# Kernel optimization log

Hardware: AMD Instinct MI355X
Metric: run time of the kernel (lower is better)

## Reference

```python
import jax, jax.numpy as jnp
import numpy as np

N_HEAD = 16
NEG_BIG = 1e10

def setup_inputs() -> dict:
    key = jax.random.key(0)
    k1, k2, k3 = jax.random.split(key, 3)
    B, S, D = 2, 2048, 1024
    x = jax.random.normal(k1, (B, S, D), dtype=jnp.float32)
    c_attn_w = jax.random.normal(k2, (D, 3 * D), dtype=jnp.float32) * 0.02
    c_attn_b = jnp.zeros((3 * D,), dtype=jnp.float32)
    c_proj_w = jax.random.normal(k3, (D, D), dtype=jnp.float32) * 0.02
    c_proj_b = jnp.zeros((D,), dtype=jnp.float32)
    return {"x": x, "c_attn_w": c_attn_w, "c_attn_b": c_attn_b,
            "c_proj_w": c_proj_w, "c_proj_b": c_proj_b}

def reference(x, c_attn_w, c_attn_b, c_proj_w, c_proj_b):
    B, S, D = x.shape
    H = N_HEAD
    hd = D // H
    # Conv1D c_attn: x @ W + b -> (B, S, 3D)
    qkv = x @ c_attn_w + c_attn_b
    q, k, v = jnp.split(qkv, 3, axis=-1)
    # split heads -> (B, H, S, hd)
    q = q.reshape(B, S, H, hd).transpose(0, 2, 1, 3)
    k = k.reshape(B, S, H, hd).transpose(0, 2, 1, 3)
    v = v.reshape(B, S, H, hd).transpose(0, 2, 1, 3)
    # QK^T with scale (scale=True)
    w = jnp.einsum('bhqd,bhkd->bhqk', q, k) / jnp.sqrt(jnp.float32(hd))
    # additive/multiplicative causal mask, exactly as source: w*b - 1e10*(1-b)
    b = jnp.tril(jnp.ones((S, S), dtype=w.dtype))
    w = w * b - NEG_BIG * (1.0 - b)
    w = jax.nn.softmax(w, axis=-1)
    a = jnp.einsum('bhqk,bhkd->bhqd', w, v)
    # merge heads -> (B, S, D)
    a = a.transpose(0, 2, 1, 3).reshape(B, S, D)
    # Conv1D c_proj
    a = a @ c_proj_w + c_proj_b
    # present = stack(key (as (B,H,S,hd)), value)
    present = jnp.stack((k, v))
    return (a, present)
```

## Files before the change

### kernel.cpp

```cpp
#include <hip/hip_runtime.h>
#include <hip/hip_bf16.h>
#include <string.h>

#define BB 2
#define SS 2048
#define DD 1024
#define NH 16
#define TT (BB * SS)
#define N3 (3 * DD)
#define A_SIZE (TT * DD)
#define PRESENT_HALF (BB * NH * SS * 64)
#define C2Q 0.18033688011112043f
#define NKT 32

typedef __attribute__((ext_vector_type(8))) short short8;
typedef __attribute__((ext_vector_type(4))) float floatx4;
typedef __attribute__((ext_vector_type(8))) unsigned short ushort8;

__device__ __forceinline__ unsigned short f2bf(float f) {
    union { float f; unsigned u; } v; v.f = f;
    unsigned r = v.u + 0x7fffu + ((v.u >> 16) & 1u);
    return (unsigned short)(r >> 16);
}
__device__ __forceinline__ unsigned pack2bf(float a, float b) {
    __hip_bfloat162 h = __float22bfloat162_rn(float2{a, b});
    unsigned u; memcpy(&u, &h, 4); return u;
}
__device__ __forceinline__ float bf2f(unsigned short u) {
    union { unsigned u; float f; } v; v.u = ((unsigned)u) << 16; return v.f;
}

__device__ __forceinline__ void async16(const unsigned short* g, unsigned short* lds) {
    __builtin_amdgcn_global_load_lds(
        (const __attribute__((address_space(1))) unsigned int*)g,
        (__attribute__((address_space(3))) unsigned int*)lds,
        16, 0, 0);
}

__global__ __launch_bounds__(256) void cast_x_kernel(const float* __restrict__ src,
                                                     unsigned short* __restrict__ dst) {
    int i = (blockIdx.x * 256 + threadIdx.x) * 8;
    float4 a = *(const float4*)(src + i);
    float4 b = *(const float4*)(src + i + 4);
    ushort8 o;
    o[0] = f2bf(a.x); o[1] = f2bf(a.y); o[2] = f2bf(a.z); o[3] = f2bf(a.w);
    o[4] = f2bf(b.x); o[5] = f2bf(b.y); o[6] = f2bf(b.z); o[7] = f2bf(b.w);
    *(ushort8*)(dst + i) = o;
}

__global__ __launch_bounds__(256) void transpose_cast_kernel(const float* __restrict__ src,
                                                             unsigned short* __restrict__ dst,
                                                             int R, int C) {
    __shared__ float tile[32][33];
    int c0 = blockIdx.x * 32, r0 = blockIdx.y * 32;
    int tx = threadIdx.x, ty = threadIdx.y;
    for (int i = ty; i < 32; i += 8)
        tile[i][tx] = src[(size_t)(r0 + i) * C + c0 + tx];
    __syncthreads();
    for (int i = ty; i < 32; i += 8)
        dst[(size_t)(c0 + i) * R + r0 + tx] = f2bf(tile[tx][i]);
}

__global__ __launch_bounds__(256)
void pv_kernel(const unsigned short* __restrict__ qkv,
               unsigned short* __restrict__ vT,
               float* __restrict__ out) {
    __shared__ unsigned short tile[64][72];
    const int bh = blockIdx.x, st = blockIdx.y;
    const int b = bh >> 4, h = bh & 15;
    const int tid = threadIdx.x;
    const int r = tid >> 2, c = (tid & 3) * 16;
    const size_t row = (size_t)(b * SS + st * 64 + r);

    const unsigned short* srcv = qkv + row * 3072 + 2048 + h * 64 + c;
    ushort8 v0 = *(const ushort8*)(srcv);
    ushort8 v1 = *(const ushort8*)(srcv + 8);
    *(ushort8*)(&tile[r][c])     = v0;
    *(ushort8*)(&tile[r][c + 8]) = v1;
    float* dv = out + A_SIZE + PRESENT_HALF + ((size_t)bh * SS + st * 64 + r) * 64 + c;
    float4 f;
    f = {bf2f(v0[0]), bf2f(v0[1]), bf2f(v0[2]), bf2f(v0[3])}; *(float4*)(dv)      = f;
    f = {bf2f(v0[4]), bf2f(v0[5]), bf2f(v0[6]), bf2f(v0[7])}; *(float4*)(dv + 4)  = f;
    f = {bf2f(v1[0]), bf2f(v1[1]), bf2f(v1[2]), bf2f(v1[3])}; *(float4*)(dv + 8)  = f;
    f = {bf2f(v1[4]), bf2f(v1[5]), bf2f(v1[6]), bf2f(v1[7])}; *(float4*)(dv + 12) = f;

    const unsigned short* srck = qkv + row * 3072 + 1024 + h * 64 + c;
    ushort8 k0 = *(const ushort8*)(srck);
    ushort8 k1 = *(const ushort8*)(srck + 8);
    float* dk = out + A_SIZE + ((size_t)bh * SS + st * 64 + r) * 64 + c;
    f = {bf2f(k0[0]), bf2f(k0[1]), bf2f(k0[2]), bf2f(k0[3])}; *(float4*)(dk)      = f;
    f = {bf2f(k0[4]), bf2f(k0[5]), bf2f(k0[6]), bf2f(k0[7])}; *(float4*)(dk + 4)  = f;
    f = {bf2f(k1[0]), bf2f(k1[1]), bf2f(k1[2]), bf2f(k1[3])}; *(float4*)(dk + 8)  = f;
    f = {bf2f(k1[4]), bf2f(k1[5]), bf2f(k1[6]), bf2f(k1[7])}; *(float4*)(dk + 12) = f;

    __syncthreads();
    const int d = tid >> 2, s0 = (tid & 3) * 16;
    unsigned short tmp[16];
    for (int e = 0; e < 16; ++e) tmp[e] = tile[s0 + e][d];
    unsigned short* dst = vT + ((size_t)bh * 64 + d) * SS + st * 64 + s0;
    *(int4*)(dst)     = *(const int4*)(tmp);
    *(int4*)(dst + 8) = *(const int4*)(tmp + 8);
}

__global__ __launch_bounds__(256, 3)
void gemm_kernel(const unsigned short* __restrict__ A,
                 const unsigned short* __restrict__ Bt,
                 const float* __restrict__ bias,
                 int mode,
                 unsigned short* __restrict__ out_bf,
                 float* __restrict__ out_f) {
    __shared__ unsigned short As3[3][8][512];
    __shared__ unsigned short Bs3[3][8][512];
    const int tid = threadIdx.x;
    const int wave = tid >> 6, lane = tid & 63;
    const int l15 = lane & 15, quad = lane >> 4;
    const int wm = wave >> 1, wn = wave & 1;
    const int t0 = blockIdx.y * 128;
    const int n0 = blockIdx.x * 128;

    floatx4 acc[4][4];
    #pragma unroll
    for (int i = 0; i < 4; ++i)
        #pragma unroll
        for (int j = 0; j < 4; ++j)
            #pragma unroll
            for (int e = 0; e < 4; ++e) acc[i][j][e] = 0.f;

    const unsigned short* gA = A  + (size_t)(t0 + wave * 32 + l15) * 1024 + quad * 8;
    const unsigned short* gB = Bt + (size_t)(n0 + wave * 32 + l15) * 1024 + quad * 8;

    #define STAGE(buf_, koff_) {                                        \
        async16(gA + (koff_),             &As3[buf_][wave * 2][0]);     \
        async16(gA + (koff_) + 16 * 1024, &As3[buf_][wave * 2 + 1][0]); \
        async16(gB + (koff_),             &Bs3[buf_][wave * 2][0]);     \
        async16(gB + (koff_) + 16 * 1024, &Bs3[buf_][wave * 2 + 1][0]); }

    STAGE(0, 0);
    STAGE(1, 32);
    asm volatile("s_waitcnt vmcnt(4)" ::: "memory");
    __builtin_amdgcn_s_barrier();
    asm volatile("" ::: "memory");

    int cur = 0, nx2 = 2;
    for (int t = 0; t < NKT; ++t) {
        if (t < NKT - 2) STAGE(nx2, (t + 2) * 32);

        const unsigned short* aB = &As3[cur][wm * 4][0] + lane * 8;
        const unsigned short* bB = &Bs3[cur][wn * 4][0] + lane * 8;
        short8 af[4], bfr[4];
        #pragma unroll
        for (int mt = 0; mt < 4; ++mt) af[mt]  = *(const short8*)(aB + mt * 512);
        #pragma unroll
        for (int nt = 0; nt < 4; ++nt) bfr[nt] = *(const short8*)(bB + nt * 512);

        __builtin_amdgcn_s_setprio(1);
        #pragma unroll
        for (int mt = 0; mt < 4; ++mt)
            #pragma unroll
            for (int nt = 0; nt < 4; ++nt)
                acc[mt][nt] = __builtin_amdgcn_mfma_f32_16x16x32_bf16(bfr[nt], af[mt], acc[mt][nt], 0, 0, 0);
        __builtin_amdgcn_s_setprio(0);

        asm volatile("s_waitcnt lgkmcnt(0)" ::: "memory");
        if (t < NKT - 2) { asm volatile("s_waitcnt vmcnt(4)" ::: "memory"); }
        else             { asm volatile("s_waitcnt vmcnt(0)" ::: "memory"); }
        asm volatile("" ::: "memory");
        __builtin_amdgcn_s_barrier();
        asm volatile("" ::: "memory");

        cur = (cur == 2) ? 0 : cur + 1;
        nx2 = (nx2 == 2) ? 0 : nx2 + 1;
    }
    #undef STAGE

    const float qs = (mode == 0 && n0 < 1024) ? C2Q : 1.0f;
    #pragma unroll
    for (int mt = 0; mt < 4; ++mt) {
        const int t = t0 + wm * 64 + mt * 16 + l15;
        if (mode == 0) {
            unsigned short* po = out_bf + (size_t)t * 3072 + n0 + wn * 64;
            #pragma unroll
            for (int nt = 0; nt < 4; ++nt) {
                float4 b4 = *(const float4*)(bias + n0 + wn * 64 + nt * 16 + quad * 4);
                float v0 = (acc[mt][nt][0] + b4.x) * qs;
                float v1 = (acc[mt][nt][1] + b4.y) * qs;
                float v2 = (acc[mt][nt][2] + b4.z) * qs;
                float v3 = (acc[mt][nt][3] + b4.w) * qs;
                uint2 w = {pack2bf(v0, v1), pack2bf(v2, v3)};
                *(uint2*)(po + nt * 16 + quad * 4) = w;
            }
        } else {
            float* po = out_f + (size_t)t * 1024 + n0 + wn * 64;
            #pragma unroll
            for (int nt = 0; nt < 4; ++nt) {
                float4 b4 = *(const float4*)(bias + n0 + wn * 64 + nt * 16 + quad * 4);
                float4 v = {acc[mt][nt][0] + b4.x, acc[mt][nt][1] + b4.y,
                            acc[mt][nt][2] + b4.z, acc[mt][nt][3] + b4.w};
                *(float4*)(po + nt * 16 + quad * 4) = v;
            }
        }
    }
}

__global__ __launch_bounds__(256)
void flash_kernel(const unsigned short* __restrict__ qkv,
                  const unsigned short* __restrict__ vT,
                  unsigned short* __restrict__ out) {
    __shared__ unsigned short Kt[2][64][72];
    __shared__ unsigned short Vt[2][64][72];
    __shared__ unsigned short Pt[4][16][72];

    const int bh = blockIdx.x;
    const int qt = 31 - blockIdx.y;
    const int b = bh >> 4, h = bh & 15;
    const int tid = threadIdx.x;
    const int wave = tid >> 6, lane = tid & 63;
    const int l15 = lane & 15, quad = lane >> 4;

    const size_t rowb = (size_t)b * SS;
    const int kcol = 1024 + h * 64;

    short8 bq0, bq1;
    {
        const unsigned short* qp = qkv + (rowb + qt * 64 + wave * 16 + l15) * 3072 + h * 64 + quad * 8;
        bq0 = *(const short8*)(qp);
        bq1 = *(const short8*)(qp + 32);
    }

    float l_i = 0.f;
    floatx4 o[4];
    for (int dt = 0; dt < 4; ++dt)
        for (int e = 0; e < 4; ++e) o[dt][e] = 0.f;

    const int qrow_l = wave * 16 + l15;

    const int rr = tid >> 3, seg = (tid & 7) * 8;
    const int vr = tid >> 2, vc = (tid & 3) * 16;
    const unsigned short* kb = qkv + rowb * 3072 + kcol;
    const unsigned short* vb = vT + (size_t)bh * 64 * SS;
    int4 ka0, ka1, va0, va1;

    #define PREF(j) { \
        const unsigned short* ks = kb + (size_t)((j) * 64 + rr) * 3072 + seg; \
        ka0 = *(const int4*)(ks); \
        ka1 = *(const int4*)(ks + 32 * 3072); \
        const unsigned short* vs = vb + (size_t)vr * SS + (j) * 64 + vc; \
        va0 = *(const int4*)(vs); \
        va1 = *(const int4*)(vs + 8); }
    #define STAGE(bf_) { \
        *(int4*)(&Kt[bf_][rr][seg])      = ka0; \
        *(int4*)(&Kt[bf_][rr + 32][seg]) = ka1; \
        *(int4*)(&Vt[bf_][vr][vc])       = va0; \
        *(int4*)(&Vt[bf_][vr][vc + 8])   = va1; }

    PREF(0);
    STAGE(0);
    if (qt > 0) PREF(1);

    for (int j = 0; j <= qt; ++j) {
        const int cur = j & 1;
        __syncthreads();
        if (j < qt) {
            STAGE(cur ^ 1);
            if (j + 2 <= qt) PREF(j + 2);
        }

        floatx4 sc[4];
        for (int nt = 0; nt < 4; ++nt)
            for (int e = 0; e < 4; ++e) sc[nt][e] = 0.f;
        __builtin_amdgcn_s_setprio(1);
        for (int nt = 0; nt < 4; ++nt) {
            const unsigned short* kp = &Kt[cur][nt * 16 + l15][quad * 8];
            short8 ak0 = *(const short8*)(kp);
            short8 ak1 = *(const short8*)(kp + 32);
            sc[nt] = __builtin_amdgcn_mfma_f32_16x16x32_bf16(ak0, bq0, sc[nt], 0, 0, 0);
            sc[nt] = __builtin_amdgcn_mfma_f32_16x16x32_bf16(ak1, bq1, sc[nt], 0, 0, 0);
        }
        __builtin_amdgcn_s_setprio(0);
        if (j == qt) {
            for (int nt = 0; nt < 4; ++nt)
                for (int r = 0; r < 4; ++r)
                    if (nt * 16 + quad * 4 + r > qrow_l) sc[nt][r] = -1.0e30f;
        }

        for (int nt = 0; nt < 4; ++nt)
            for (int r = 0; r < 4; ++r) {
                float p = __builtin_amdgcn_exp2f(sc[nt][r]);
                sc[nt][r] = p;
                l_i += p;
            }

        for (int nt = 0; nt < 4; ++nt) {
            uint2 w = {pack2bf(sc[nt][0], sc[nt][1]), pack2bf(sc[nt][2], sc[nt][3])};
            *(uint2*)(&Pt[wave][l15][nt * 16 + quad * 4]) = w;
        }
        asm volatile("s_waitcnt lgkmcnt(0)" ::: "memory");
        short8 bp0 = *(const short8*)(&Pt[wave][l15][quad * 8]);
        short8 bp1 = *(const short8*)(&Pt[wave][l15][32 + quad * 8]);
        __builtin_amdgcn_s_setprio(1);
        for (int dt = 0; dt < 4; ++dt) {
            const unsigned short* vp = &Vt[cur][dt * 16 + l15][quad * 8];
            short8 av0 = *(const short8*)(vp);
            short8 av1 = *(const short8*)(vp + 32);
            o[dt] = __builtin_amdgcn_mfma_f32_16x16x32_bf16(av0, bp0, o[dt], 0, 0, 0);
            o[dt] = __builtin_amdgcn_mfma_f32_16x16x32_bf16(av1, bp1, o[dt], 0, 0, 0);
        }
        __builtin_amdgcn_s_setprio(0);
    }
    #undef PREF
    #undef STAGE

    l_i += __shfl_xor(l_i, 16);
    l_i += __shfl_xor(l_i, 32);
    float inv = 1.f / l_i;
    const int qrow = qt * 64 + wave * 16 + l15;
    unsigned short* po = out + (rowb + qrow) * 1024 + h * 64;
    for (int dt = 0; dt < 4; ++dt) {
        uint2 w = {pack2bf(o[dt][0] * inv, o[dt][1] * inv),
                   pack2bf(o[dt][2] * inv, o[dt][3] * inv)};
        *(uint2*)(po + dt * 16 + quad * 4) = w;
    }
}

extern "C" void kernel_launch(void* const* d_in, const int* in_sizes, int n_in,
                              void* d_out, int out_size, void* d_ws, size_t ws_size,
                              hipStream_t stream) {
    const float* x        = (const float*)d_in[0];
    const float* c_attn_w = (const float*)d_in[1];
    const float* c_attn_b = (const float*)d_in[2];
    const float* c_proj_w = (const float*)d_in[3];
    const float* c_proj_b = (const float*)d_in[4];
    float* out = (float*)d_out;

    char* ws = (char*)d_ws;
    unsigned short* xb     = (unsigned short*)(ws);
    unsigned short* wqkvt  = (unsigned short*)(ws + 8388608);
    unsigned short* wprojt = (unsigned short*)(ws + 14680064);
    unsigned short* qkvb   = (unsigned short*)(ws + 16777216);
    unsigned short* aout   = (unsigned short*)(ws + 41943040);
    unsigned short* vT     = xb;

    cast_x_kernel<<<(TT * DD) / (256 * 8), 256, 0, stream>>>(x, xb);
    transpose_cast_kernel<<<dim3(N3 / 32, DD / 32), dim3(32, 8), 0, stream>>>(c_attn_w, wqkvt, DD, N3);
    transpose_cast_kernel<<<dim3(DD / 32, DD / 32), dim3(32, 8), 0, stream>>>(c_proj_w, wprojt, DD, DD);
    gemm_kernel<<<dim3(N3 / 128, TT / 128), 256, 0, stream>>>(xb, wqkvt, c_attn_b, 0, qkvb, nullptr);
    pv_kernel<<<dim3(32, 32), 256, 0, stream>>>(qkvb, vT, out);
    flash_kernel<<<dim3(32, 32), 256, 0, stream>>>(qkvb, vT, aout);
    gemm_kernel<<<dim3(DD / 128, TT / 128), 256, 0, stream>>>(aout, wprojt, c_proj_b, 1, nullptr, out);
}
```

Baseline: 240.3 us.

## Split GEMM into QKV and proj kernels with XCD-aware tile remap

Replaces the shared triple-buffered GEMM with two specialised kernels. The QKV GEMM drops to double buffering with plain __syncthreads and remaps block indices so tiles landing on the same XCD share rows and columns, aiming for better L2 reuse. The projection GEMM moves to 64x64 tiles, giving 1024 blocks instead of 256 for fuller CU coverage, and uses a similar XCD swizzle. The trade-off is less prefetch depth, losing the setprio and explicit waitcnt tuning, and lower per-block arithmetic intensity in the projection.

```diff
diff --git a/kernel.cpp b/kernel.cpp
--- a/kernel.cpp
+++ b/kernel.cpp
@@ -102,21 +102,24 @@
     *(int4*)(dst + 8) = *(const int4*)(tmp + 8);
 }
 
-__global__ __launch_bounds__(256, 3)
-void gemm_kernel(const unsigned short* __restrict__ A,
-                 const unsigned short* __restrict__ Bt,
-                 const float* __restrict__ bias,
-                 int mode,
-                 unsigned short* __restrict__ out_bf,
-                 float* __restrict__ out_f) {
-    __shared__ unsigned short As3[3][8][512];
-    __shared__ unsigned short Bs3[3][8][512];
+__global__ __launch_bounds__(256)
+void gemm_qkv_kernel(const unsigned short* __restrict__ A,
+                     const unsigned short* __restrict__ Bt,
+                     const float* __restrict__ bias,
+                     unsigned short* __restrict__ out_bf) {
+    __shared__ unsigned short As[2][8][512];
+    __shared__ unsigned short Bs[2][8][512];
     const int tid = threadIdx.x;
     const int wave = tid >> 6, lane = tid & 63;
     const int l15 = lane & 15, quad = lane >> 4;
     const int wm = wave >> 1, wn = wave & 1;
-    const int t0 = blockIdx.y * 128;
-    const int n0 = blockIdx.x * 128;
+
+    const int d_  = blockIdx.y * 24 + blockIdx.x;
+    const int xcd = d_ & 7, li = d_ >> 3;
+    const int tx  = (xcd & 1) * 12 + li % 12;
+    const int ty  = (xcd >> 1) * 8 + li / 12;
+    const int t0 = ty * 128;
+    const int n0 = tx * 128;
 
     floatx4 acc[4][4];
     #pragma unroll
@@ -130,74 +133,117 @@
     const unsigned short* gB = Bt + (size_t)(n0 + wave * 32 + l15) * 1024 + quad * 8;
 
     #define STAGE(buf_, koff_) {                                        \
-        async16(gA + (koff_),             &As3[buf_][wave * 2][0]);     \
-        async16(gA + (koff_) + 16 * 1024, &As3[buf_][wave * 2 + 1][0]); \
-        async16(gB + (koff_),             &Bs3[buf_][wave * 2][0]);     \
-        async16(gB + (koff_) + 16 * 1024, &Bs3[buf_][wave * 2 + 1][0]); }
+        async16(gA + (koff_),             &As[buf_][wave * 2][0]);      \
+        async16(gA + (koff_) + 16 * 1024, &As[buf_][wave * 2 + 1][0]);  \
+        async16(gB + (koff_),             &Bs[buf_][wave * 2][0]);      \
+        async16(gB + (koff_) + 16 * 1024, &Bs[buf_][wave * 2 + 1][0]); }
 
     STAGE(0, 0);
-    STAGE(1, 32);
-    asm volatile("s_waitcnt vmcnt(4)" ::: "memory");
-    __builtin_amdgcn_s_barrier();
-    asm volatile("" ::: "memory");
-
-    int cur = 0, nx2 = 2;
-    for (int t = 0; t < NKT; ++t) {
-        if (t < NKT - 2) STAGE(nx2, (t + 2) * 32);
-
-        const unsigned short* aB = &As3[cur][wm * 4][0] + lane * 8;
-        const unsigned short* bB = &Bs3[cur][wn * 4][0] + lane * 8;
+
+    for (int kt = 0; kt < NKT; ++kt) {
+        const int cur = kt & 1;
+        __syncthreads();
+        if (kt < NKT - 1) STAGE(cur ^ 1, (kt + 1) * 32);
+
+        const unsigned short* aB = &As[cur][wm * 4][0] + lane * 8;
+        const unsigned short* bB = &Bs[cur][wn * 4][0] + lane * 8;
         short8 af[4], bfr[4];
         #pragma unroll
         for (int mt = 0; mt < 4; ++mt) af[mt]  = *(const short8*)(aB + mt * 512);
         #pragma unroll
         for (int nt = 0; nt < 4; ++nt) bfr[nt] = *(const short8*)(bB + nt * 512);
-
-        __builtin_amdgcn_s_setprio(1);
         #pragma unroll
         for (int mt = 0; mt < 4; ++mt)
             #pragma unroll
             for (int nt = 0; nt < 4; ++nt)
                 acc[mt][nt] = __builtin_amdgcn_mfma_f32_16x16x32_bf16(bfr[nt], af[mt], acc[mt][nt], 0, 0, 0);
-        __builtin_amdgcn_s_setprio(0);
-
-        asm volatile("s_waitcnt lgkmcnt(0)" ::: "memory");
-        if (t < NKT - 2) { asm volatile("s_waitcnt vmcnt(4)" ::: "memory"); }
-        else             { asm volatile("s_waitcnt vmcnt(0)" ::: "memory"); }
-        asm volatile("" ::: "memory");
-        __builtin_amdgcn_s_barrier();
-        asm volatile("" ::: "memory");
-
-        cur = (cur == 2) ? 0 : cur + 1;
-        nx2 = (nx2 == 2) ? 0 : nx2 + 1;
     }
     #undef STAGE
 
-    const float qs = (mode == 0 && n0 < 1024) ? C2Q : 1.0f;
+    const float qs = (n0 < 1024) ? C2Q : 1.0f;
     #pragma unroll
     for (int mt = 0; mt < 4; ++mt) {
         const int t = t0 + wm * 64 + mt * 16 + l15;
-        if (mode == 0) {
-            unsigned short* po = out_bf + (size_t)t * 3072 + n0 + wn * 64;
+        unsigned short* po = out_bf + (size_t)t * 3072 + n0 + wn * 64;
+        #pragma unroll
+        for (int nt = 0; nt < 4; ++nt) {
+            float4 b4 = *(const float4*)(bias + n0 + wn * 64 + nt * 16 + quad * 4);
+            float v0 = (acc[mt][nt][0] + b4.x) * qs;
+            float v1 = (acc[mt][nt][1] + b4.y) * qs;
+            float v2 = (acc[mt][nt][2] + b4.z) * qs;
+            float v3 = (acc[mt][nt][3] + b4.w) * qs;
+            uint2 w = {pack2bf(v0, v1), pack2bf(v2, v3)};
+            *(uint2*)(po + nt * 16 + quad * 4) = w;
+        }
+    }
+}
+
+__global__ __launch_bounds__(256)
+void gemm_proj_kernel(const unsigned short* __restrict__ A,
+                      const unsigned short* __restrict__ Bt,
+                      const float* __restrict__ bias,
+                      float* __restrict__ out_f) {
+    __shared__ unsigned short As[2][4][512];
+    __shared__ unsigned short Bs[2][4][512];
+    const int tid = threadIdx.x;
+    const int wave = tid >> 6, lane = tid & 63;
+    const int l15 = lane & 15, quad = lane >> 4;
+    const int wm = wave >> 1, wn = wave & 1;
+
+    const int d_  = blockIdx.y * 16 + blockIdx.x;
+    const int xcd = d_ & 7, li = d_ >> 3;
+    const int tx  = (xcd & 1) * 8 + (li & 7);
+    const int ty  = (xcd >> 1) * 16 + (li >> 3);
+    const int t0 = ty * 64;
+    const int n0 = tx * 64;
+
+    floatx4 acc[2][2];
+    #pragma unroll
+    for (int i = 0; i < 2; ++i)
+        #pragma unroll
+        for (int j = 0; j < 2; ++j)
             #pragma unroll
-            for (int nt = 0; nt < 4; ++nt) {
-                float4 b4 = *(const float4*)(bias + n0 + wn * 64 + nt * 16 + quad * 4);
-                float v0 = (acc[mt][nt][0] + b4.x) * qs;
-                float v1 = (acc[mt][nt][1] + b4.y) * qs;
-                float v2 = (acc[mt][nt][2] + b4.z) * qs;
-                float v3 = (acc[mt][nt][3] + b4.w) * qs;
-                uint2 w = {pack2bf(v0, v1), pack2bf(v2, v3)};
-                *(uint2*)(po + nt * 16 + quad * 4) = w;
-            }
-        } else {
-            float* po = out_f + (size_t)t * 1024 + n0 + wn * 64;
+            for (int e = 0; e < 4; ++e) acc[i][j][e] = 0.f;
+
+    const unsigned short* gA = A  + (size_t)(t0 + wave * 16 + l15) * 1024 + quad * 8;
+    const unsigned short* gB = Bt + (size_t)(n0 + wave * 16 + l15) * 1024 + quad * 8;
+
+    #define STAGE(buf_, koff_) {                          \
+        async16(gA + (koff_), &As[buf_][wave][0]);        \
+        async16(gB + (koff_), &Bs[buf_][wave][0]); }
+
+    STAGE(0, 0);
+
+    for (int kt = 0; kt < NKT; ++kt) {
+        const int cur = kt & 1;
+        __syncthreads();
+        if (kt < NKT - 1) STAGE(cur ^ 1, (kt + 1) * 32);
+
+        const unsigned short* aB = &As[cur][wm * 2][0] + lane * 8;
+        const unsigned short* bB = &Bs[cur][wn * 2][0] + lane * 8;
+        short8 af[2], bfr[2];
+        af[0]  = *(const short8*)(aB);
+        af[1]  = *(const short8*)(aB + 512);
+        bfr[0] = *(const short8*)(bB);
+        bfr[1] = *(const short8*)(bB + 512);
+        #pragma unroll
+        for (int mt = 0; mt < 2; ++mt)
             #pragma unroll
-            for (int nt = 0; nt < 4; ++nt) {
-                float4 b4 = *(const float4*)(bias + n0 + wn * 64 + nt * 16 + quad * 4);
-                float4 v = {acc[mt][nt][0] + b4.x, acc[mt][nt][1] + b4.y,
-                            acc[mt][nt][2] + b4.z, acc[mt][nt][3] + b4.w};
-                *(float4*)(po + nt * 16 + quad * 4) = v;
-            }
+            for (int nt = 0; nt < 2; ++nt)
+                acc[mt][nt] = __builtin_amdgcn_mfma_f32_16x16x32_bf16(bfr[nt], af[mt], acc[mt][nt], 0, 0, 0);
+    }
+    #undef STAGE
+
+    #pragma unroll
+    for (int mt = 0; mt < 2; ++mt) {
+        const int t = t0 + wm * 32 + mt * 16 + l15;
+        float* po = out_f + (size_t)t * 1024 + n0 + wn * 32;
+        #pragma unroll
+        for (int nt = 0; nt < 2; ++nt) {
+            float4 b4 = *(const float4*)(bias + n0 + wn * 32 + nt * 16 + quad * 4);
+            float4 v = {acc[mt][nt][0] + b4.x, acc[mt][nt][1] + b4.y,
+                        acc[mt][nt][2] + b4.z, acc[mt][nt][3] + b4.w};
+            *(float4*)(po + nt * 16 + quad * 4) = v;
         }
     }
 }
@@ -343,8 +389,8 @@
     cast_x_kernel<<<(TT * DD) / (256 * 8), 256, 0, stream>>>(x, xb);
     transpose_cast_kernel<<<dim3(N3 / 32, DD / 32), dim3(32, 8), 0, stream>>>(c_attn_w, wqkvt, DD, N3);
     transpose_cast_kernel<<<dim3(DD / 32, DD / 32), dim3(32, 8), 0, stream>>>(c_proj_w, wprojt, DD, DD);
-    gemm_kernel<<<dim3(N3 / 128, TT / 128), 256, 0, stream>>>(xb, wqkvt, c_attn_b, 0, qkvb, nullptr);
+    gemm_qkv_kernel<<<dim3(N3 / 128, TT / 128), 256, 0, stream>>>(xb, wqkvt, c_attn_b, qkvb);
     pv_kernel<<<dim3(32, 32), 256, 0, stream>>>(qkvb, vT, out);
     flash_kernel<<<dim3(32, 32), 256, 0, stream>>>(qkvb, vT, aout);
-    gemm_kernel<<<dim3(DD / 128, TT / 128), 256, 0, stream>>>(aout, wprojt, c_proj_b, 1, nullptr, out);
-}
+    gemm_proj_kernel<<<dim3(DD / 64, TT / 64), 256, 0, stream>>>(aout, wprojt, c_proj_b, out);
+}
```

Measured after the change: 237.4 us. Within noise of the previous version (-1.2%).
